# Kernel tuning notes

Measured on AMD Instinct MI355X. Metric: run time of the kernel, lower is better.

## Reference

```python
import jax, jax.numpy as jnp
import numpy as np

DIM, HEADS, HD, FFN = 1536, 12, 128, 8960
B, F, H, W = 1, 4, 20, 32
S = F * H * W          # 2560 latent tokens
L2 = 512               # text context length
EPS = 1e-6


def _ln(x):
    m = jnp.mean(x, -1, keepdims=True)
    v = jnp.mean(jnp.square(x - m), -1, keepdims=True)
    return (x - m) * jax.lax.rsqrt(v + EPS)


def _rms(x, g):
    return x * jax.lax.rsqrt(jnp.mean(jnp.square(x), -1, keepdims=True) + EPS) * g


def _dyn_quant(x):
    # per-token symmetric int8 dynamic activation quantization (A8, dynamic input scale)
    s = jnp.maximum(jnp.max(jnp.abs(x), -1, keepdims=True) / 127.0, 1e-8)
    q = jnp.clip(jnp.round(x / s), -127.0, 127.0)
    return q, s, jnp.sum(q, -1)   # sum_input used for asymmetric-weight zero-point correction


def _quant_w(w):
    # per-output-channel asymmetric int8 weight quantization (weight_sym=False)
    wmin = jnp.min(w, 1, keepdims=True)
    wmax = jnp.max(w, 1, keepdims=True)
    s = jnp.maximum((wmax - wmin) / 255.0, 1e-8)
    zp = jnp.round(-128.0 - wmin / s)
    qw = jnp.clip(jnp.round(w / s) + zp, -128.0, 127.0)
    return qw, s[:, 0], zp[:, 0]


def _w8a8(qx, s_x, sum_qx, w, b):
    # y = s_x * s_w * (qx @ (qw - zp)^T) + b = s_x*s_w*(qx@qw^T - zp*sum(qx)) + b
    qw, sw, zp = _quant_w(w)
    acc = jnp.einsum('bsi,oi->bso', qx, qw) - sum_qx[..., None] * zp
    return acc * s_x * sw + b


def _rope(x, fr, f, h, w):
    # x: [B,S,N,D] with S == f*h*w; fr: [1024, D//2] complex rope table
    Bn, Sn, N, D = x.shape
    c = D // 2
    s0 = c - 2 * (c // 3)
    fF = jnp.broadcast_to(fr[:f, :s0].reshape(f, 1, 1, s0), (f, h, w, s0))
    fH = jnp.broadcast_to(fr[:h, s0:s0 + c // 3].reshape(1, h, 1, c // 3), (f, h, w, c // 3))
    fW = jnp.broadcast_to(fr[:w, s0 + c // 3:].reshape(1, 1, w, c // 3), (f, h, w, c // 3))
    fi = jnp.concatenate([fF, fH, fW], -1).reshape(1, f * h * w, 1, c)
    xr = x.reshape(Bn, Sn, N, c, 2)
    xc = jax.lax.complex(xr[..., 0], xr[..., 1]) * fi
    return jnp.stack([jnp.real(xc), jnp.imag(xc)], -1).reshape(Bn, Sn, N, D)


def _attn(q, k, v, k_lens):
    scale = 1.0 / jnp.sqrt(jnp.float32(q.shape[-1]))
    scores = jnp.einsum('bqnd,bknd->bnqk', q, k) * scale
    mask = jnp.arange(k.shape[1])[None, None, None, :] < k_lens[:, None, None, None]
    p = jax.nn.softmax(jnp.where(mask, scores, -1e30), -1)
    return jnp.einsum('bnqk,bknd->bqnd', p, v)


def _forward(x, e, freqs, context, modulation,
             wq, bq, wk, bk, wv, bv, wo, bo, gq, gk, n3_w, n3_b,
             cwq, cbq, cwk, cbk, cwv, cbv, cwo, cbo, cgq, cgk,
             w1, b1, w2, b2, f, h, w, seq_lens, context_lens):
    fr = jax.lax.complex(freqs[..., 0], freqs[..., 1])
    em = modulation + e  # [B,6,C]
    sm, sc, gm, smlp, scmlp, gmlp = [em[:, i:i + 1] for i in range(6)]
    Bn, Sn, C = x.shape
    # --- self attention: fused norm+modulation then shared per-token int8 quant for q/k/v ---
    h1 = _ln(x) * (1.0 + sc) + sm
    qx, s_x, sum_qx = _dyn_quant(h1)
    q = _rms(_w8a8(qx, s_x, sum_qx, wq, bq), gq).reshape(Bn, Sn, HEADS, HD)
    k = _rms(_w8a8(qx, s_x, sum_qx, wk, bk), gk).reshape(Bn, Sn, HEADS, HD)
    v = _w8a8(qx, s_x, sum_qx, wv, bv).reshape(Bn, Sn, HEADS, HD)
    q = _rope(q, fr, f, h, w)
    k = _rope(k, fr, f, h, w)
    y = _attn(q, k, v, seq_lens).reshape(Bn, Sn, C) @ wo.T + bo
    x = x + y * gm
    # --- cross attention (fp16/fp path in the original; use_kernel[1]=False) ---
    hx = _ln(x) * n3_w + n3_b
    cq = _rms(hx @ cwq.T + cbq, cgq).reshape(Bn, Sn, HEADS, HD)
    ck = _rms(context @ cwk.T + cbk, cgk).reshape(Bn, L2, HEADS, HD)
    cv = (context @ cwv.T + cbv).reshape(Bn, L2, HEADS, HD)
    y = _attn(cq, ck, cv, context_lens).reshape(Bn, Sn, C) @ cwo.T + cbo
    x = x + y
    # --- FFN with modulation (use_kernel[2]=False) ---
    h2 = _ln(x) * (1.0 + scmlp) + smlp
    y = jax.nn.gelu(h2 @ w1.T + b1, approximate=True) @ w2.T + b2
    return x + y * gmlp


def setup_inputs():
    key = jax.random.key(0)
    ks = jax.random.split(key, 16)

    def P(i, shape, s=0.02):
        return jax.random.normal(ks[i], shape, jnp.float32) * s

    x = jax.random.normal(ks[0], (B, S, DIM), jnp.float32)
    e = jax.random.normal(ks[1], (B, 6, DIM), jnp.float32)
    context = jax.random.normal(ks[2], (B, L2, DIM), jnp.float32)
    seq_lens = jnp.array([S], jnp.int32)
    grid_sizes = jnp.array([[F, H, W]], jnp.int32)
    context_lens = jnp.array([L2], jnp.int32)
    c = HD // 2
    pos = np.arange(1024, dtype=np.float64)[:, None]
    theta = 1.0 / (10000.0 ** (np.arange(c, dtype=np.float64) / c))
    ang = pos * theta
    freqs = jnp.asarray(np.stack([np.cos(ang), np.sin(ang)], -1), jnp.float32)
    z = lambda n: jnp.zeros((n,), jnp.float32)
    o = lambda n: jnp.ones((n,), jnp.float32)
    return dict(x=x, e=e, seq_lens=seq_lens, grid_sizes=grid_sizes, freqs=freqs,
                context=context, context_lens=context_lens,
                modulation=P(3, (1, 6, DIM), 1.0 / DIM ** 0.5),
                wq=P(4, (DIM, DIM)), bq=z(DIM), wk=P(5, (DIM, DIM)), bk=z(DIM),
                wv=P(6, (DIM, DIM)), bv=z(DIM), wo=P(7, (DIM, DIM)), bo=z(DIM),
                gq=o(DIM), gk=o(DIM), n3_w=o(DIM), n3_b=z(DIM),
                cwq=P(8, (DIM, DIM)), cbq=z(DIM), cwk=P(9, (DIM, DIM)), cbk=z(DIM),
                cwv=P(10, (DIM, DIM)), cbv=z(DIM), cwo=P(11, (DIM, DIM)), cbo=z(DIM),
                cgq=o(DIM), cgk=o(DIM),
                w1=P(12, (FFN, DIM)), b1=z(FFN), w2=P(13, (DIM, FFN)), b2=z(DIM))


def reference(x, e, seq_lens, grid_sizes, freqs, context, context_lens, modulation,
              wq, bq, wk, bk, wv, bv, wo, bo, gq, gk, n3_w, n3_b,
              cwq, cbq, cwk, cbk, cwv, cbv, cwo, cbo, cgq, cgk,
              w1, b1, w2, b2):
    f, h, w = int(grid_sizes[0, 0]), int(grid_sizes[0, 1]), int(grid_sizes[0, 2])
    return _forward(x, e, freqs, context, modulation,
                    wq, bq, wk, bk, wv, bv, wo, bo, gq, gk, n3_w, n3_b,
                    cwq, cbq, cwk, cbk, cwv, cbv, cwo, cbo, cgq, cgk,
                    w1, b1, w2, b2, f, h, w, seq_lens, context_lens)
```

## Files before the change

### kernel.cpp

```cpp
#include <hip/hip_runtime.h>
#include <stdint.h>


typedef unsigned short u16;
typedef __bf16 bf16x8 __attribute__((ext_vector_type(8)));
typedef float f32x4 __attribute__((ext_vector_type(4)));

#define DEV __device__ __forceinline__

DEV u16 f2b(float f) {
  uint32_t u = __float_as_uint(f);
  u += 0x7fffu + ((u >> 16) & 1u);
  return (u16)(u >> 16);
}

DEV float gelu_tanh(float v) {
  float u = 0.7978845608028654f * (v + 0.044715f * v * v * v);
  return 0.5f * v * (1.0f + tanhf(u));
}

DEV void gl_lds16(const u16* g, u16* l) {
  __builtin_amdgcn_global_load_lds(
      (const __attribute__((address_space(1))) void*)g,
      (__attribute__((address_space(3))) void*)l, 16, 0, 0);
}

DEV float bred_sum(float v, float* scr) {
  #pragma unroll
  for (int o = 32; o; o >>= 1) v += __shfl_down(v, o, 64);
  if ((threadIdx.x & 63) == 0) scr[threadIdx.x >> 6] = v;
  __syncthreads();
  v = scr[0] + scr[1] + scr[2] + scr[3];
  __syncthreads();
  return v;
}
DEV float bred_max(float v, float* scr) {
  #pragma unroll
  for (int o = 32; o; o >>= 1) v = fmaxf(v, __shfl_down(v, o, 64));
  if ((threadIdx.x & 63) == 0) scr[threadIdx.x >> 6] = v;
  __syncthreads();
  v = fmaxf(fmaxf(scr[0], scr[1]), fmaxf(scr[2], scr[3]));
  __syncthreads();
  return v;
}
DEV float bred_min(float v, float* scr) {
  #pragma unroll
  for (int o = 32; o; o >>= 1) v = fminf(v, __shfl_down(v, o, 64));
  if ((threadIdx.x & 63) == 0) scr[threadIdx.x >> 6] = v;
  __syncthreads();
  v = fminf(fminf(scr[0], scr[1]), fminf(scr[2], scr[3]));
  __syncthreads();
  return v;
}

__global__ __launch_bounds__(256) void pack_kernel(
    const float* __restrict__ e, const float* __restrict__ mod,
    const float* __restrict__ cbk, const float* __restrict__ cbv,
    float* __restrict__ em, float* __restrict__ bckv) {
  int i = blockIdx.x * 256 + threadIdx.x;
  if (i < 9216) em[i] = e[i] + mod[i];
  if (i < 3072) bckv[i] = (i < 1536) ? cbk[i] : cbv[i - 1536];
}

__global__ __launch_bounds__(256) void cvt_bf16_kernel(
    const float* __restrict__ in, u16* __restrict__ out, int n4) {
  int stride = gridDim.x * 256;
  for (int i = blockIdx.x * 256 + threadIdx.x; i < n4; i += stride) {
    float4 v = ((const float4*)in)[i];
    uint2 r;
    r.x = (uint32_t)f2b(v.x) | ((uint32_t)f2b(v.y) << 16);
    r.y = (uint32_t)f2b(v.z) | ((uint32_t)f2b(v.w) << 16);
    ((uint2*)out)[i] = r;
  }
}

__global__ __launch_bounds__(256) void ln_quant_kernel(
    const float* __restrict__ x, const float* __restrict__ em,
    u16* __restrict__ qx, float* __restrict__ sx, float* __restrict__ sumq) {
  __shared__ float scr[4];
  const int row = blockIdx.x, tid = threadIdx.x;
  const float* xr = x + (size_t)row * 1536;
  float v[6], s = 0.f, s2 = 0.f;
  #pragma unroll
  for (int t = 0; t < 6; t++) { v[t] = xr[tid + t * 256]; s += v[t]; s2 += v[t] * v[t]; }
  s = bred_sum(s, scr); s2 = bred_sum(s2, scr);
  float mean = s / 1536.f;
  float var = s2 / 1536.f - mean * mean;
  float inv = rsqrtf(var + 1e-6f);
  float hv[6], amax = 0.f;
  #pragma unroll
  for (int t = 0; t < 6; t++) {
    int i = tid + t * 256;
    hv[t] = (v[t] - mean) * inv * (1.f + em[1536 + i]) + em[i];
    amax = fmaxf(amax, fabsf(hv[t]));
  }
  amax = bred_max(amax, scr);
  float sxv = fmaxf(amax / 127.f, 1e-8f);
  float qs = 0.f;
  #pragma unroll
  for (int t = 0; t < 6; t++) {
    int i = tid + t * 256;
    float q = fminf(fmaxf(rintf(hv[t] / sxv), -127.f), 127.f);
    qs += q;
    qx[(size_t)row * 1536 + i] = f2b(q);
  }
  qs = bred_sum(qs, scr);
  if (tid == 0) { sx[row] = sxv; sumq[row] = qs; }
}

__global__ __launch_bounds__(256) void quantw_kernel(
    const float* __restrict__ wq, const float* __restrict__ wk, const float* __restrict__ wv,
    const float* __restrict__ bq, const float* __restrict__ bk, const float* __restrict__ bv,
    u16* __restrict__ qw, float* __restrict__ sw, float* __restrict__ zp, float* __restrict__ ball) {
  __shared__ float scr[4];
  const int row = blockIdx.x, tid = threadIdx.x;
  const int sel = (row >= 3072) ? 2 : (row >= 1536 ? 1 : 0);
  const int r = row - sel * 1536;
  const float* w = sel == 0 ? wq : (sel == 1 ? wk : wv);
  const float* bb = sel == 0 ? bq : (sel == 1 ? bk : bv);
  const float* wr = w + (size_t)r * 1536;
  float v[6], mn = 1e30f, mx = -1e30f;
  #pragma unroll
  for (int t = 0; t < 6; t++) { v[t] = wr[tid + t * 256]; mn = fminf(mn, v[t]); mx = fmaxf(mx, v[t]); }
  mn = bred_min(mn, scr); mx = bred_max(mx, scr);
  float s = fmaxf((mx - mn) / 255.f, 1e-8f);
  float z = rintf(-128.f - mn / s);
  #pragma unroll
  for (int t = 0; t < 6; t++) {
    int i = tid + t * 256;
    float q = fminf(fmaxf(rintf(v[t] / s) + z, -128.f), 127.f);
    qw[(size_t)row * 1536 + i] = f2b(q);
  }
  if (tid == 0) { sw[row] = s; zp[row] = z; ball[row] = bb[r]; }
}

template<int EP>
DEV void gemm_epilogue(float v, int row, int col, int N, void* Cout,
                       const float* bias, const float* sxp, const float* sumqp,
                       const float* swp, const float* zpp,
                       const float* gp, const float* residp) {
  size_t idx = (size_t)row * N + col;
  if constexpr (EP == 0) {
    ((float*)Cout)[idx] = v + bias[col];
  } else if constexpr (EP == 1) {
    v = (v - sumqp[row] * zpp[col]) * (sxp[row] * swp[col]) + bias[col];
    ((float*)Cout)[idx] = v;
  } else if constexpr (EP == 2) {
    v += bias[col];
    if (gp) v *= gp[col];
    ((float*)Cout)[idx] = v + residp[idx];
  } else {
    ((u16*)Cout)[idx] = f2b(gelu_tanh(v + bias[col]));
  }
}

template<int EP>
__global__ __launch_bounds__(256) void gemm_bt_kernel(
    const u16* __restrict__ A, const u16* __restrict__ B, void* __restrict__ Cout,
    int N, int K, const float* __restrict__ bias,
    const float* __restrict__ sxp, const float* __restrict__ sumqp,
    const float* __restrict__ swp, const float* __restrict__ zpp,
    const float* __restrict__ gp, const float* __restrict__ residp) {
  __shared__ __align__(16) u16 As[128 * 32];
  __shared__ __align__(16) u16 Bs[128 * 32];
  const int tid = threadIdx.x;
  const int wave = tid >> 6, lane = tid & 63;
  const int wm = wave >> 1, wn = wave & 1;
  const int quad = lane >> 4, l16 = lane & 15;
  const int m0 = blockIdx.y * 128, n0 = blockIdx.x * 128;

  int srow[2], scol[2];
  #pragma unroll
  for (int i = 0; i < 2; i++) {
    int row = (wave * 2 + i) * 16 + (lane >> 2);
    int chunk = ((lane & 3) - (row >> 1)) & 3;
    srow[i] = row; scol[i] = chunk * 8;
  }

  f32x4 acc[4][4];
  #pragma unroll
  for (int i = 0; i < 4; i++)
    #pragma unroll
    for (int j = 0; j < 4; j++) acc[i][j] = (f32x4){0.f, 0.f, 0.f, 0.f};

  for (int k0 = 0; k0 < K; k0 += 32) {
    #pragma unroll
    for (int i = 0; i < 2; i++) {
      gl_lds16(A + (size_t)(m0 + srow[i]) * K + k0 + scol[i], &As[(wave * 2 + i) * 512]);
      gl_lds16(B + (size_t)(n0 + srow[i]) * K + k0 + scol[i], &Bs[(wave * 2 + i) * 512]);
    }
    __syncthreads();
    bf16x8 af[4], bfv[4];
    #pragma unroll
    for (int mi = 0; mi < 4; mi++) {
      int row = wm * 64 + mi * 16 + l16;
      af[mi] = *(const bf16x8*)&As[row * 32 + (((quad + (row >> 1)) & 3) * 8)];
    }
    #pragma unroll
    for (int ni = 0; ni < 4; ni++) {
      int row = wn * 64 + ni * 16 + l16;
      bfv[ni] = *(const bf16x8*)&Bs[row * 32 + (((quad + (row >> 1)) & 3) * 8)];
    }
    #pragma unroll
    for (int mi = 0; mi < 4; mi++)
      #pragma unroll
      for (int ni = 0; ni < 4; ni++)
        acc[mi][ni] = __builtin_amdgcn_mfma_f32_16x16x32_bf16(af[mi], bfv[ni], acc[mi][ni], 0, 0, 0);
    __syncthreads();
  }
  #pragma unroll
  for (int mi = 0; mi < 4; mi++)
    #pragma unroll
    for (int ni = 0; ni < 4; ni++) {
      int col = n0 + wn * 64 + ni * 16 + l16;
      #pragma unroll
      for (int r = 0; r < 4; r++)
        gemm_epilogue<EP>(acc[mi][ni][r], m0 + wm * 64 + mi * 16 + quad * 4 + r, col,
                          N, Cout, bias, sxp, sumqp, swp, zpp, gp, residp);
    }
}

template<int EP>
__global__ __launch_bounds__(256) void gemm64_bt_kernel(
    const u16* __restrict__ A, const u16* __restrict__ B, void* __restrict__ Cout,
    int N, int K, const float* __restrict__ bias,
    const float* __restrict__ sxp, const float* __restrict__ sumqp,
    const float* __restrict__ swp, const float* __restrict__ zpp,
    const float* __restrict__ gp, const float* __restrict__ residp) {
  __shared__ __align__(16) u16 As[2][64 * 32];
  __shared__ __align__(16) u16 Bs[2][128 * 32];
  const int tid = threadIdx.x;
  const int wave = tid >> 6, lane = tid & 63;
  const int quad = lane >> 4, l16 = lane & 15;
  const int m0 = blockIdx.y * 64, n0 = blockIdx.x * 128;

  const int arow = wave * 16 + (lane >> 2);
  const int acol = (((lane & 3) - (arow >> 1)) & 3) * 8;
  int brow[2], bcol[2];
  #pragma unroll
  for (int i = 0; i < 2; i++) {
    int row = (wave * 2 + i) * 16 + (lane >> 2);
    brow[i] = row; bcol[i] = (((lane & 3) - (row >> 1)) & 3) * 8;
  }

  f32x4 acc[8];
  #pragma unroll
  for (int i = 0; i < 8; i++) acc[i] = (f32x4){0.f, 0.f, 0.f, 0.f};

  const int nk = K >> 5;
  gl_lds16(A + (size_t)(m0 + arow) * K + acol, &As[0][wave * 512]);
  #pragma unroll
  for (int i = 0; i < 2; i++)
    gl_lds16(B + (size_t)(n0 + brow[i]) * K + bcol[i], &Bs[0][(wave * 2 + i) * 512]);

  for (int kt = 0; kt < nk; kt++) {
    __syncthreads();
    const int cur = kt & 1;
    if (kt + 1 < nk) {
      const int k0n = (kt + 1) << 5;
      gl_lds16(A + (size_t)(m0 + arow) * K + k0n + acol, &As[1 - cur][wave * 512]);
      #pragma unroll
      for (int i = 0; i < 2; i++)
        gl_lds16(B + (size_t)(n0 + brow[i]) * K + k0n + bcol[i], &Bs[1 - cur][(wave * 2 + i) * 512]);
    }
    const int ar = wave * 16 + l16;
    bf16x8 af = *(const bf16x8*)&As[cur][ar * 32 + (((quad + (ar >> 1)) & 3) * 8)];
    #pragma unroll
    for (int ni = 0; ni < 8; ni++) {
      int row = ni * 16 + l16;
      bf16x8 bf = *(const bf16x8*)&Bs[cur][row * 32 + (((quad + (row >> 1)) & 3) * 8)];
      acc[ni] = __builtin_amdgcn_mfma_f32_16x16x32_bf16(af, bf, acc[ni], 0, 0, 0);
    }
  }
  #pragma unroll
  for (int ni = 0; ni < 8; ni++) {
    int col = n0 + ni * 16 + l16;
    #pragma unroll
    for (int r = 0; r < 4; r++)
      gemm_epilogue<EP>(acc[ni][r], m0 + wave * 16 + quad * 4 + r, col,
                        N, Cout, bias, sxp, sumqp, swp, zpp, gp, residp);
  }
}

__global__ __launch_bounds__(256) void rmsrope_b_kernel(
    const float* __restrict__ qkv, u16* __restrict__ qkvb,
    const float* __restrict__ gq, const float* __restrict__ gk,
    const float* __restrict__ freqs, const int* __restrict__ gsz) {
  __shared__ float scr[4];
  const int row = blockIdx.x, tid = threadIdx.x;
  const float* base = qkv + (size_t)row * 4608;
  u16* ob = qkvb + (size_t)row * 4608;
  const int gh = gsz[1], gw = gsz[2];
  const int hw = gh * gw;
  const int fi = row / hw, rem = row - fi * hw;
  const int hi = rem / gw, wi = rem - hi * gw;
  #pragma unroll
  for (int part = 0; part < 2; part++) {
    const float* p = base + part * 1536;
    u16* o = ob + part * 1536;
    const float* g = part ? gk : gq;
    const float sc = part ? 1.f : 0.08838834764831845f;
    float v[6], s2 = 0.f;
    #pragma unroll
    for (int t = 0; t < 6; t++) { v[t] = p[tid + t * 256]; s2 += v[t] * v[t]; }
    s2 = bred_sum(s2, scr);
    float inv = rsqrtf(s2 / 1536.f + 1e-6f);
    #pragma unroll
    for (int t = 0; t < 3; t++) {
      int pr = tid + t * 256;
      int c = pr & 63;
      int frow = (c < 22) ? fi : (c < 43 ? hi : wi);
      const float* fr = freqs + ((size_t)frow * 64 + c) * 2;
      float cv = fr[0], sv = fr[1];
      float x0 = p[2 * pr] * inv * g[2 * pr];
      float x1 = p[2 * pr + 1] * inv * g[2 * pr + 1];
      o[2 * pr] = f2b((x0 * cv - x1 * sv) * sc);
      o[2 * pr + 1] = f2b((x0 * sv + x1 * cv) * sc);
    }
  }
  #pragma unroll
  for (int t = 0; t < 6; t++) {
    int i = tid + t * 256;
    ob[3072 + i] = f2b(base[3072 + i]);
  }
}

__global__ __launch_bounds__(256) void rms_bf16_kernel(
    const float* __restrict__ X, u16* __restrict__ O, const float* __restrict__ g,
    int ldi, int ldo, float scale) {
  __shared__ float scr[4];
  const int row = blockIdx.x, tid = threadIdx.x;
  const float* xr = X + (size_t)row * ldi;
  u16* orow = O + (size_t)row * ldo;
  float v[6], s2 = 0.f;
  #pragma unroll
  for (int t = 0; t < 6; t++) { v[t] = xr[tid + t * 256]; s2 += v[t] * v[t]; }
  s2 = bred_sum(s2, scr);
  float inv = rsqrtf(s2 / 1536.f + 1e-6f) * scale;
  #pragma unroll
  for (int t = 0; t < 6; t++) {
    int i = tid + t * 256;
    orow[i] = f2b(v[t] * inv * g[i]);
  }
}

__global__ __launch_bounds__(256) void vtrans_kernel(
    const float* __restrict__ V, int ld, u16* __restrict__ Vt, int Skv) {
  __shared__ u16 T[64 * 136];
  const int h = blockIdx.y, k0 = blockIdx.x * 64, tid = threadIdx.x;
  #pragma unroll
  for (int i = 0; i < 8; i++) {
    int f4 = i * 256 + tid;
    int row = f4 >> 5, c4 = f4 & 31;
    float4 v = *(const float4*)(V + (size_t)(k0 + row) * ld + h * 128 + c4 * 4);
    ushort4 b;
    b.x = f2b(v.x); b.y = f2b(v.y); b.z = f2b(v.z); b.w = f2b(v.w);
    *(ushort4*)&T[row * 136 + c4 * 4] = b;
  }
  __syncthreads();
  #pragma unroll
  for (int i = 0; i < 4; i++) {
    int f8 = i * 256 + tid;
    int hd = f8 >> 3, kc = f8 & 7;
    u16 tmp[8];
    #pragma unroll
    for (int j = 0; j < 8; j++) tmp[j] = T[(kc * 8 + j) * 136 + hd];
    *(uint4*)(Vt + ((size_t)h * 128 + hd) * Skv + k0 + kc * 8) = *(const uint4*)tmp;
  }
}

__global__ __launch_bounds__(256) void fattn_kernel(
    const u16* __restrict__ Q, int ldq, const u16* __restrict__ Kg, int ldk,
    const u16* __restrict__ Vtg, u16* __restrict__ O, int ldo,
    const int* __restrict__ klen_ptr, int kmax) {
  __shared__ __align__(16) u16 Qs[64 * 136];
  __shared__ __align__(16) u16 Ks[64 * 136];
  __shared__ __align__(16) u16 Vt[128 * 72];
  __shared__ __align__(16) u16 Pt[4][16 * 72];
  const int tid = threadIdx.x, wave = tid >> 6, lane = tid & 63;
  const int quad = lane >> 4, l16 = lane & 15;
  const int h = blockIdx.y;
  const int q0 = blockIdx.x * 64;
  int klen = klen_ptr[0]; if (klen > kmax) klen = kmax;
  const u16* vbase = Vtg + (size_t)h * 128 * kmax;

  #pragma unroll
  for (int i = 0; i < 4; i++) {
    int c8 = i * 256 + tid;
    int row = c8 >> 4, cc = (c8 & 15) * 8;
    *(uint4*)&Qs[row * 136 + cc] = *(const uint4*)(Q + (size_t)(q0 + row) * ldq + h * 128 + cc);
  }
  __syncthreads();
  bf16x8 qf[4];
  #pragma unroll
  for (int s = 0; s < 4; s++)
    qf[s] = *(const bf16x8*)&Qs[(wave * 16 + l16) * 136 + s * 32 + quad * 8];

  float m_r[4] = {-1e30f, -1e30f, -1e30f, -1e30f};
  float l_r[4] = {0.f, 0.f, 0.f, 0.f};
  f32x4 oacc[8];
  #pragma unroll
  for (int n8 = 0; n8 < 8; n8++) oacc[n8] = (f32x4){0.f, 0.f, 0.f, 0.f};

  const int ktiles = (klen + 63) >> 6;
  for (int kt = 0; kt < ktiles; kt++) {
    const int k0 = kt * 64;
    __syncthreads();
    #pragma unroll
    for (int i = 0; i < 4; i++) {
      int c8 = i * 256 + tid;
      int row = c8 >> 4, cc = (c8 & 15) * 8;
      *(uint4*)&Ks[row * 136 + cc] = *(const uint4*)(Kg + (size_t)(k0 + row) * ldk + h * 128 + cc);
    }
    #pragma unroll
    for (int i = 0; i < 4; i++) {
      int f8 = i * 256 + tid;
      int hd = f8 >> 3, kc = f8 & 7;
      *(uint4*)&Vt[hd * 72 + kc * 8] = *(const uint4*)(vbase + (size_t)hd * kmax + k0 + kc * 8);
    }
    __syncthreads();
    f32x4 sacc[4];
    #pragma unroll
    for (int ni = 0; ni < 4; ni++) sacc[ni] = (f32x4){0.f, 0.f, 0.f, 0.f};
    #pragma unroll
    for (int ni = 0; ni < 4; ni++)
      #pragma unroll
      for (int s = 0; s < 4; s++) {
        bf16x8 kf = *(const bf16x8*)&Ks[(ni * 16 + l16) * 136 + s * 32 + quad * 8];
        sacc[ni] = __builtin_amdgcn_mfma_f32_16x16x32_bf16(qf[s], kf, sacc[ni], 0, 0, 0);
      }
    float alpha_r[4];
    #pragma unroll
    for (int r = 0; r < 4; r++) {
      float mx = -1e30f;
      #pragma unroll
      for (int ni = 0; ni < 4; ni++) {
        int col = k0 + ni * 16 + l16;
        float sv = (col < klen) ? sacc[ni][r] : -1e30f;
        sacc[ni][r] = sv;
        mx = fmaxf(mx, sv);
      }
      #pragma unroll
      for (int off = 1; off < 16; off <<= 1) mx = fmaxf(mx, __shfl_xor(mx, off, 64));
      float mnew = fmaxf(m_r[r], mx);
      float alpha = __expf(m_r[r] - mnew);
      float rsum = 0.f;
      float pv[4];
      #pragma unroll
      for (int ni = 0; ni < 4; ni++) {
        float p = __expf(sacc[ni][r] - mnew);
        pv[ni] = p;
        rsum += p;
      }
      #pragma unroll
      for (int off = 1; off < 16; off <<= 1) rsum += __shfl_xor(rsum, off, 64);
      l_r[r] = l_r[r] * alpha + rsum;
      m_r[r] = mnew;
      alpha_r[r] = alpha;
      #pragma unroll
      for (int ni = 0; ni < 4; ni++)
        Pt[wave][(quad * 4 + r) * 72 + ni * 16 + l16] = f2b(pv[ni]);
    }
    #pragma unroll
    for (int n8 = 0; n8 < 8; n8++)
      #pragma unroll
      for (int r = 0; r < 4; r++) oacc[n8][r] *= alpha_r[r];
    #pragma unroll
    for (int s2 = 0; s2 < 2; s2++) {
      bf16x8 pf = *(const bf16x8*)&Pt[wave][l16 * 72 + s2 * 32 + quad * 8];
      #pragma unroll
      for (int n8 = 0; n8 < 8; n8++) {
        bf16x8 vf = *(const bf16x8*)&Vt[(n8 * 16 + l16) * 72 + s2 * 32 + quad * 8];
        oacc[n8] = __builtin_amdgcn_mfma_f32_16x16x32_bf16(pf, vf, oacc[n8], 0, 0, 0);
      }
    }
  }
  float rl[4];
  #pragma unroll
  for (int r = 0; r < 4; r++) rl[r] = 1.f / l_r[r];
  #pragma unroll
  for (int n8 = 0; n8 < 8; n8++)
    #pragma unroll
    for (int r = 0; r < 4; r++) {
      int row = q0 + wave * 16 + quad * 4 + r;
      O[(size_t)row * ldo + h * 128 + n8 * 16 + l16] = f2b(oacc[n8][r] * rl[r]);
    }
}

__global__ __launch_bounds__(256) void ln_affine_kernel(
    const float* __restrict__ X, u16* __restrict__ O,
    const float* __restrict__ w, const float* __restrict__ b, float addone) {
  __shared__ float scr[4];
  const int row = blockIdx.x, tid = threadIdx.x;
  const float* xr = X + (size_t)row * 1536;
  float v[6], s = 0.f, s2 = 0.f;
  #pragma unroll
  for (int t = 0; t < 6; t++) { v[t] = xr[tid + t * 256]; s += v[t]; s2 += v[t] * v[t]; }
  s = bred_sum(s, scr); s2 = bred_sum(s2, scr);
  float mean = s / 1536.f;
  float inv = rsqrtf(s2 / 1536.f - mean * mean + 1e-6f);
  #pragma unroll
  for (int t = 0; t < 6; t++) {
    int i = tid + t * 256;
    O[(size_t)row * 1536 + i] = f2b((v[t] - mean) * inv * (addone + w[i]) + b[i]);
  }
}

extern "C" void kernel_launch(void* const* d_in, const int* in_sizes, int n_in,
                              void* d_out, int out_size, void* d_ws, size_t ws_size,
                              hipStream_t stream) {
  (void)in_sizes; (void)n_in; (void)out_size; (void)ws_size;
  const int S = 2560, D = 1536, L2C = 512, FF = 8960, ND = 4608, CKV = 3072;

  const float* x = (const float*)d_in[0];
  const float* e = (const float*)d_in[1];
  const int* seq_lens = (const int*)d_in[2];
  const int* grid_sz = (const int*)d_in[3];
  const float* freqs = (const float*)d_in[4];
  const float* context = (const float*)d_in[5];
  const int* ctx_lens = (const int*)d_in[6];
  const float* modulation = (const float*)d_in[7];
  const float* wq = (const float*)d_in[8];  const float* bq = (const float*)d_in[9];
  const float* wk = (const float*)d_in[10]; const float* bk = (const float*)d_in[11];
  const float* wv = (const float*)d_in[12]; const float* bv = (const float*)d_in[13];
  const float* wo = (const float*)d_in[14]; const float* bo = (const float*)d_in[15];
  const float* gq = (const float*)d_in[16]; const float* gk = (const float*)d_in[17];
  const float* n3w = (const float*)d_in[18]; const float* n3b = (const float*)d_in[19];
  const float* cwq = (const float*)d_in[20]; const float* cbq = (const float*)d_in[21];
  const float* cwk = (const float*)d_in[22]; const float* cbk = (const float*)d_in[23];
  const float* cwv = (const float*)d_in[24]; const float* cbv = (const float*)d_in[25];
  const float* cwo = (const float*)d_in[26]; const float* cbo = (const float*)d_in[27];
  const float* cgq = (const float*)d_in[28]; const float* cgk = (const float*)d_in[29];
  const float* w1 = (const float*)d_in[30]; const float* b1 = (const float*)d_in[31];
  const float* w2 = (const float*)d_in[32]; const float* b2 = (const float*)d_in[33];

  char* wsb = (char*)d_ws;
  size_t off = 0;
  auto alloc = [&](size_t bytes) -> void* {
    void* r = wsb + off;
    off += (bytes + 255) & ~(size_t)255;
    return r;
  };
  float* em   = (float*)alloc((size_t)6 * D * 4);
  float* bckv = (float*)alloc((size_t)CKV * 4);
  float* ball = (float*)alloc((size_t)ND * 4);
  float* sx   = (float*)alloc((size_t)S * 4);
  float* sumq = (float*)alloc((size_t)S * 4);
  float* sw   = (float*)alloc((size_t)ND * 4);
  float* zp   = (float*)alloc((size_t)ND * 4);
  u16* qx     = (u16*)alloc((size_t)S * D * 2);
  u16* qw     = (u16*)alloc((size_t)ND * D * 2);
  float* qkv  = (float*)alloc((size_t)S * ND * 4);
  u16* qkvb   = (u16*)alloc((size_t)S * ND * 2);
  u16* attnb  = (u16*)alloc((size_t)S * D * 2);
  u16* hx     = (u16*)alloc((size_t)S * D * 2);
  float* cq   = (float*)alloc((size_t)S * D * 4);
  float* ckv  = (float*)alloc((size_t)L2C * CKV * 4);
  u16* ctxb   = (u16*)alloc((size_t)L2C * D * 2);
  u16* cattn  = (u16*)alloc((size_t)S * D * 2);
  u16* wo_b   = (u16*)alloc((size_t)D * D * 2);
  u16* cwq_b  = (u16*)alloc((size_t)D * D * 2);
  u16* cwkv_b = (u16*)alloc((size_t)2 * D * D * 2);
  u16* cwo_b  = (u16*)alloc((size_t)D * D * 2);
  u16* w1_b   = (u16*)alloc((size_t)FF * D * 2);
  u16* w2_b   = (u16*)alloc((size_t)D * FF * 2);
  u16* h3 = (u16*)qkv;
  u16* h2 = attnb;
  u16* vtg = qw;
  u16* cvtg = qx;
  u16* cqb = hx;
  u16* ckvb = ctxb;
  float* x2 = cq;
  float* x1 = (float*)d_out;
  float* outp = (float*)d_out;

  auto cvt = [&](const float* in, u16* op, size_t n) {
    int n4 = (int)(n / 4);
    int blocks = (n4 + 255) / 256; if (blocks > 4096) blocks = 4096;
    cvt_bf16_kernel<<<blocks, 256, 0, stream>>>(in, op, n4);
  };

  pack_kernel<<<36, 256, 0, stream>>>(e, modulation, cbk, cbv, em, bckv);
  cvt(wo, wo_b, (size_t)D * D);
  cvt(cwq, cwq_b, (size_t)D * D);
  cvt(cwk, cwkv_b, (size_t)D * D);
  cvt(cwv, cwkv_b + (size_t)D * D, (size_t)D * D);
  cvt(cwo, cwo_b, (size_t)D * D);
  cvt(w1, w1_b, (size_t)FF * D);
  cvt(w2, w2_b, (size_t)D * FF);
  cvt(context, ctxb, (size_t)L2C * D);

  ln_quant_kernel<<<S, 256, 0, stream>>>(x, em, qx, sx, sumq);
  quantw_kernel<<<ND, 256, 0, stream>>>(wq, wk, wv, bq, bk, bv, qw, sw, zp, ball);

  gemm_bt_kernel<1><<<dim3(ND / 128, S / 128), 256, 0, stream>>>(
      qx, qw, qkv, ND, D, ball, sx, sumq, sw, zp, nullptr, nullptr);

  rmsrope_b_kernel<<<S, 256, 0, stream>>>(qkv, qkvb, gq, gk, freqs, grid_sz);
  vtrans_kernel<<<dim3(S / 64, 12), 256, 0, stream>>>(qkv + 3072, ND, vtg, S);

  fattn_kernel<<<dim3(S / 64, 12), 256, 0, stream>>>(
      qkvb, ND, qkvb + 1536, ND, vtg, attnb, D, seq_lens, S);

  gemm64_bt_kernel<2><<<dim3(D / 128, S / 64), 256, 0, stream>>>(
      attnb, wo_b, x1, D, D, bo, nullptr, nullptr, nullptr, nullptr, em + 2 * D, x);

  ln_affine_kernel<<<S, 256, 0, stream>>>(x1, hx, n3w, n3b, 0.f);

  gemm64_bt_kernel<0><<<dim3(D / 128, S / 64), 256, 0, stream>>>(
      hx, cwq_b, cq, D, D, cbq, nullptr, nullptr, nullptr, nullptr, nullptr, nullptr);
  gemm64_bt_kernel<0><<<dim3(CKV / 128, L2C / 64), 256, 0, stream>>>(
      ctxb, cwkv_b, ckv, CKV, D, bckv, nullptr, nullptr, nullptr, nullptr, nullptr, nullptr);

  rms_bf16_kernel<<<S, 256, 0, stream>>>(cq, cqb, cgq, D, D, 0.08838834764831845f);
  rms_bf16_kernel<<<L2C, 256, 0, stream>>>(ckv, ckvb, cgk, CKV, D, 1.f);
  vtrans_kernel<<<dim3(L2C / 64, 12), 256, 0, stream>>>(ckv + 1536, CKV, cvtg, L2C);

  fattn_kernel<<<dim3(S / 64, 12), 256, 0, stream>>>(
      cqb, D, ckvb, D, cvtg, cattn, D, ctx_lens, L2C);

  gemm64_bt_kernel<2><<<dim3(D / 128, S / 64), 256, 0, stream>>>(
      cattn, cwo_b, x2, D, D, cbo, nullptr, nullptr, nullptr, nullptr, nullptr, x1);

  ln_affine_kernel<<<S, 256, 0, stream>>>(x2, h2, em + 4 * D, em + 3 * D, 1.f);

  gemm_bt_kernel<3><<<dim3(FF / 128, S / 128), 256, 0, stream>>>(
      h2, w1_b, h3, FF, D, b1, nullptr, nullptr, nullptr, nullptr, nullptr, nullptr);

  gemm64_bt_kernel<2><<<dim3(D / 128, S / 64), 256, 0, stream>>>(
      h3, w2_b, outp, D, FF, b2, nullptr, nullptr, nullptr, nullptr, em + 5 * D, x2);
}
```

Baseline: 1.013 ms.

## Use BK=64 with 2x2 wave tiling in gemm64 and split-K the FFN down-projection

The 64x128 GEMM kernel now stages 64-wide K tiles and arranges its four waves in a 2x2 grid with 2x4 MFMA tiles per wave. This raises fragment reuse and halves the number of barriers per K. The final FFN down-projection (K=8960) is split into two K halves across blockIdx.z, writing fp32 partials into reused scratch buffers. A separate reduce kernel then adds bias, gate and residual. This doubles the block count for the long-K GEMM to improve occupancy, at the cost of extra partial-result traffic and an additional launch.

Result: faster. 939.3 us (-7.2%).

```diff
diff --git a/kernel.cpp b/kernel.cpp
--- a/kernel.cpp
+++ b/kernel.cpp
@@ -149,8 +149,10 @@
     v += bias[col];
     if (gp) v *= gp[col];
     ((float*)Cout)[idx] = v + residp[idx];
+  } else if constexpr (EP == 3) {
+    ((u16*)Cout)[idx] = f2b(gelu_tanh(v + bias[col]));
   } else {
-    ((u16*)Cout)[idx] = f2b(gelu_tanh(v + bias[col]));
+    ((float*)Cout)[idx] = v;
   }
 }
 
@@ -222,63 +224,107 @@
 
 template<int EP>
 __global__ __launch_bounds__(256) void gemm64_bt_kernel(
-    const u16* __restrict__ A, const u16* __restrict__ B, void* __restrict__ Cout,
-    int N, int K, const float* __restrict__ bias,
+    const u16* __restrict__ A, const u16* __restrict__ B,
+    void* __restrict__ Cout, void* __restrict__ Cout2, int N, int K, int KC,
+    const float* __restrict__ bias,
     const float* __restrict__ sxp, const float* __restrict__ sumqp,
     const float* __restrict__ swp, const float* __restrict__ zpp,
     const float* __restrict__ gp, const float* __restrict__ residp) {
-  __shared__ __align__(16) u16 As[2][64 * 32];
-  __shared__ __align__(16) u16 Bs[2][128 * 32];
+  __shared__ __align__(16) u16 As[2][64 * 64];
+  __shared__ __align__(16) u16 Bs[2][128 * 64];
   const int tid = threadIdx.x;
   const int wave = tid >> 6, lane = tid & 63;
+  const int wm = wave >> 1, wn = wave & 1;
   const int quad = lane >> 4, l16 = lane & 15;
   const int m0 = blockIdx.y * 64, n0 = blockIdx.x * 128;
-
-  const int arow = wave * 16 + (lane >> 2);
-  const int acol = (((lane & 3) - (arow >> 1)) & 3) * 8;
-  int brow[2], bcol[2];
+  const int kstart = blockIdx.z * KC;
+
+  int arow[2], acol[2], brow[4], bcol[4];
   #pragma unroll
   for (int i = 0; i < 2; i++) {
-    int row = (wave * 2 + i) * 16 + (lane >> 2);
-    brow[i] = row; bcol[i] = (((lane & 3) - (row >> 1)) & 3) * 8;
-  }
-
-  f32x4 acc[8];
-  #pragma unroll
-  for (int i = 0; i < 8; i++) acc[i] = (f32x4){0.f, 0.f, 0.f, 0.f};
-
-  const int nk = K >> 5;
-  gl_lds16(A + (size_t)(m0 + arow) * K + acol, &As[0][wave * 512]);
+    int row = (wave * 2 + i) * 8 + (lane >> 3);
+    arow[i] = row; acol[i] = (((lane & 7) - (row >> 1)) & 7) * 8;
+  }
+  #pragma unroll
+  for (int i = 0; i < 4; i++) {
+    int row = (wave * 4 + i) * 8 + (lane >> 3);
+    brow[i] = row; bcol[i] = (((lane & 7) - (row >> 1)) & 7) * 8;
+  }
+
+  f32x4 acc[2][4];
   #pragma unroll
   for (int i = 0; i < 2; i++)
-    gl_lds16(B + (size_t)(n0 + brow[i]) * K + bcol[i], &Bs[0][(wave * 2 + i) * 512]);
-
+    #pragma unroll
+    for (int j = 0; j < 4; j++) acc[i][j] = (f32x4){0.f, 0.f, 0.f, 0.f};
+
+  const int nk = KC >> 6;
+  auto stage = [&](int buf, int k0) {
+    #pragma unroll
+    for (int i = 0; i < 2; i++)
+      gl_lds16(A + (size_t)(m0 + arow[i]) * K + kstart + k0 + acol[i],
+               &As[buf][(wave * 2 + i) * 512]);
+    #pragma unroll
+    for (int i = 0; i < 4; i++)
+      gl_lds16(B + (size_t)(n0 + brow[i]) * K + kstart + k0 + bcol[i],
+               &Bs[buf][(wave * 4 + i) * 512]);
+  };
+  stage(0, 0);
   for (int kt = 0; kt < nk; kt++) {
     __syncthreads();
     const int cur = kt & 1;
-    if (kt + 1 < nk) {
-      const int k0n = (kt + 1) << 5;
-      gl_lds16(A + (size_t)(m0 + arow) * K + k0n + acol, &As[1 - cur][wave * 512]);
-      #pragma unroll
-      for (int i = 0; i < 2; i++)
-        gl_lds16(B + (size_t)(n0 + brow[i]) * K + k0n + bcol[i], &Bs[1 - cur][(wave * 2 + i) * 512]);
-    }
-    const int ar = wave * 16 + l16;
-    bf16x8 af = *(const bf16x8*)&As[cur][ar * 32 + (((quad + (ar >> 1)) & 3) * 8)];
-    #pragma unroll
-    for (int ni = 0; ni < 8; ni++) {
-      int row = ni * 16 + l16;
-      bf16x8 bf = *(const bf16x8*)&Bs[cur][row * 32 + (((quad + (row >> 1)) & 3) * 8)];
-      acc[ni] = __builtin_amdgcn_mfma_f32_16x16x32_bf16(af, bf, acc[ni], 0, 0, 0);
-    }
-  }
-  #pragma unroll
-  for (int ni = 0; ni < 8; ni++) {
-    int col = n0 + ni * 16 + l16;
-    #pragma unroll
-    for (int r = 0; r < 4; r++)
-      gemm_epilogue<EP>(acc[ni][r], m0 + wave * 16 + quad * 4 + r, col,
-                        N, Cout, bias, sxp, sumqp, swp, zpp, gp, residp);
+    if (kt + 1 < nk) stage(1 - cur, (kt + 1) << 6);
+    #pragma unroll
+    for (int s = 0; s < 2; s++) {
+      bf16x8 af[2], bfv[4];
+      #pragma unroll
+      for (int mi = 0; mi < 2; mi++) {
+        int row = wm * 32 + mi * 16 + l16;
+        int slot = ((s * 4 + quad) + (row >> 1)) & 7;
+        af[mi] = *(const bf16x8*)&As[cur][row * 64 + slot * 8];
+      }
+      #pragma unroll
+      for (int ni = 0; ni < 4; ni++) {
+        int row = wn * 64 + ni * 16 + l16;
+        int slot = ((s * 4 + quad) + (row >> 1)) & 7;
+        bfv[ni] = *(const bf16x8*)&Bs[cur][row * 64 + slot * 8];
+      }
+      #pragma unroll
+      for (int mi = 0; mi < 2; mi++)
+        #pragma unroll
+        for (int ni = 0; ni < 4; ni++)
+          acc[mi][ni] = __builtin_amdgcn_mfma_f32_16x16x32_bf16(af[mi], bfv[ni], acc[mi][ni], 0, 0, 0);
+    }
+  }
+  void* Cuse = (EP == 4 && blockIdx.z) ? Cout2 : Cout;
+  #pragma unroll
+  for (int mi = 0; mi < 2; mi++)
+    #pragma unroll
+    for (int ni = 0; ni < 4; ni++) {
+      int col = n0 + wn * 64 + ni * 16 + l16;
+      #pragma unroll
+      for (int r = 0; r < 4; r++)
+        gemm_epilogue<EP>(acc[mi][ni][r], m0 + wm * 32 + mi * 16 + quad * 4 + r, col,
+                          N, Cuse, bias, sxp, sumqp, swp, zpp, gp, residp);
+    }
+}
+
+__global__ __launch_bounds__(256) void splitk_reduce_kernel(
+    const float* __restrict__ P0, const float* __restrict__ P1,
+    float* __restrict__ out, const float* __restrict__ bias,
+    const float* __restrict__ g, const float* __restrict__ resid,
+    int N, int n4) {
+  int stride = gridDim.x * 256;
+  for (int i = blockIdx.x * 256 + threadIdx.x; i < n4; i += stride) {
+    float4 a = ((const float4*)P0)[i];
+    float4 b = ((const float4*)P1)[i];
+    float4 r = ((const float4*)resid)[i];
+    int col = (i * 4) % N;
+    float4 o;
+    o.x = (a.x + b.x + bias[col]) * g[col] + r.x;
+    o.y = (a.y + b.y + bias[col + 1]) * g[col + 1] + r.y;
+    o.z = (a.z + b.z + bias[col + 2]) * g[col + 2] + r.z;
+    o.w = (a.w + b.w + bias[col + 3]) * g[col + 3] + r.w;
+    ((float4*)out)[i] = o;
   }
 }
 
@@ -573,6 +619,8 @@
   float* x2 = cq;
   float* x1 = (float*)d_out;
   float* outp = (float*)d_out;
+  float* P0 = (float*)qx;
+  float* P1 = (float*)qkvb;
 
   auto cvt = [&](const float* in, u16* op, size_t n) {
     int n4 = (int)(n / 4);
@@ -603,14 +651,14 @@
       qkvb, ND, qkvb + 1536, ND, vtg, attnb, D, seq_lens, S);
 
   gemm64_bt_kernel<2><<<dim3(D / 128, S / 64), 256, 0, stream>>>(
-      attnb, wo_b, x1, D, D, bo, nullptr, nullptr, nullptr, nullptr, em + 2 * D, x);
+      attnb, wo_b, x1, nullptr, D, D, D, bo, nullptr, nullptr, nullptr, nullptr, em + 2 * D, x);
 
   ln_affine_kernel<<<S, 256, 0, stream>>>(x1, hx, n3w, n3b, 0.f);
 
   gemm64_bt_kernel<0><<<dim3(D / 128, S / 64), 256, 0, stream>>>(
-      hx, cwq_b, cq, D, D, cbq, nullptr, nullptr, nullptr, nullptr, nullptr, nullptr);
+      hx, cwq_b, cq, nullptr, D, D, D, cbq, nullptr, nullptr, nullptr, nullptr, nullptr, nullptr);
   gemm64_bt_kernel<0><<<dim3(CKV / 128, L2C / 64), 256, 0, stream>>>(
-      ctxb, cwkv_b, ckv, CKV, D, bckv, nullptr, nullptr, nullptr, nullptr, nullptr, nullptr);
+      ctxb, cwkv_b, ckv, nullptr, CKV, D, D, bckv, nullptr, nullptr, nullptr, nullptr, nullptr, nullptr);
 
   rms_bf16_kernel<<<S, 256, 0, stream>>>(cq, cqb, cgq, D, D, 0.08838834764831845f);
   rms_bf16_kernel<<<L2C, 256, 0, stream>>>(ckv, ckvb, cgk, CKV, D, 1.f);
@@ -620,13 +668,15 @@
       cqb, D, ckvb, D, cvtg, cattn, D, ctx_lens, L2C);
 
   gemm64_bt_kernel<2><<<dim3(D / 128, S / 64), 256, 0, stream>>>(
-      cattn, cwo_b, x2, D, D, cbo, nullptr, nullptr, nullptr, nullptr, nullptr, x1);
+      cattn, cwo_b, x2, nullptr, D, D, D, cbo, nullptr, nullptr, nullptr, nullptr, nullptr, x1);
 
   ln_affine_kernel<<<S, 256, 0, stream>>>(x2, h2, em + 4 * D, em + 3 * D, 1.f);
 
   gemm_bt_kernel<3><<<dim3(FF / 128, S / 128), 256, 0, stream>>>(
       h2, w1_b, h3, FF, D, b1, nullptr, nullptr, nullptr, nullptr, nullptr, nullptr);
 
-  gemm64_bt_kernel<2><<<dim3(D / 128, S / 64), 256, 0, stream>>>(
-      h3, w2_b, outp, D, FF, b2, nullptr, nullptr, nullptr, nullptr, em + 5 * D, x2);
-}
+  gemm64_bt_kernel<4><<<dim3(D / 128, S / 64, 2), 256, 0, stream>>>(
+      h3, w2_b, P0, P1, D, FF, FF / 2, nullptr, nullptr, nullptr, nullptr, nullptr, nullptr, nullptr);
+  splitk_reduce_kernel<<<960, 256, 0, stream>>>(
+      P0, P1, outp, b2, em + 5 * D, x2, D, S * D / 4);
+}
```
